# Performance work log

Hardware: AMD Instinct MI355X
Metric: run time of the kernel (lower is better)

## Reference

```python
import jax, jax.numpy as jnp
import numpy as np

H, D, G, P = 8, 64, 64, 3
ROPE_BASE = 10000.0

def _gelu(x):
    return jax.nn.gelu(x, approximate=False)  # torch nn.GELU default (erf)

def setup_inputs() -> dict:
    key = jax.random.key(0)
    ks = jax.random.split(key, 20)
    B, N, C = 2, 32768, 256
    inner = H * D
    s = 0.02
    inp = {
        'x': jax.random.normal(ks[0], (B, N, C), jnp.float32),
        'pos': jax.random.uniform(ks[1], (B, N, P), jnp.float32),
        'gumbel_u': jax.random.uniform(ks[2], (B, H, N, G), jnp.float32),
        'Wx': jax.random.normal(ks[3], (C, inner), jnp.float32) * s,
        'bx': jnp.zeros((inner,), jnp.float32),
        'W1': jax.random.normal(ks[4], (D, G), jnp.float32) * s,   # proj_temperature[0]
        'b1': jnp.zeros((G,), jnp.float32),
        'W2': jax.random.normal(ks[5], (G, 1), jnp.float32) * s,   # proj_temperature[2]
        'b2': jnp.zeros((1,), jnp.float32),
        'bias': jnp.full((1, H, 1, 1), 0.5, jnp.float32),
        'Wr': jax.random.normal(ks[6], (2 * P, D), jnp.float32) * s,  # rope_projection
        'br': jnp.zeros((D,), jnp.float32),
        'Ws': jax.random.normal(ks[7], (D, G), jnp.float32) * s,   # in_project_slice
        'bs': jnp.zeros((G,), jnp.float32),
        'Wq': jax.random.normal(ks[8], (D, D), jnp.float32) * s,
        'Wk': jax.random.normal(ks[9], (D, D), jnp.float32) * s,
        'Wv': jax.random.normal(ks[10], (D, D), jnp.float32) * s,
        'Wg1': jax.random.normal(ks[11], (2 * D, D), jnp.float32) * s,  # attn_gate[0]
        'bg1': jnp.zeros((D,), jnp.float32),
        'Wg2': jax.random.normal(ks[12], (D, D), jnp.float32) * s,      # attn_gate[2]
        'bg2': jnp.zeros((D,), jnp.float32),
        'Wo': jax.random.normal(ks[13], (inner, C), jnp.float32) * s,   # to_out
        'bo': jnp.zeros((C,), jnp.float32),
    }
    return inp

def reference(x, pos, gumbel_u, Wx, bx, W1, b1, W2, b2, bias, Wr, br, Ws, bs,
              Wq, Wk, Wv, Wg1, bg1, Wg2, bg2, Wo, bo):
    B, N, C = x.shape
    dt = x.dtype
    # project and split heads: [B,H,N,D]
    x_mid = (x @ Wx + bx).reshape(B, N, H, D).transpose(0, 2, 1, 3)
    # RoPE features: sin/cos of pos * inv_freq, projected to dim_head
    inv_freq = jnp.exp(-jnp.arange(P, dtype=dt) * jnp.log(jnp.asarray(ROPE_BASE, dt)) / P)
    ang = pos[..., :P] * inv_freq                                  # [B,N,P]
    rope_feat = jnp.concatenate([jnp.sin(ang), jnp.cos(ang)], -1)  # [B,N,2P]
    x_mid = x_mid + (rope_feat @ Wr + br)[:, None]                 # broadcast over heads
    # per-token temperature, clamped
    temp = _gelu(_gelu(x_mid @ W1 + b1) @ W2 + b2) + bias          # [B,H,N,1]
    temp = jnp.maximum(temp, 0.01)
    # gumbel-softmax slice weights (soft, hard=False)
    logits = x_mid @ Ws + bs                                       # [B,H,N,G]
    gnoise = -jnp.log(-jnp.log(gumbel_u + 1e-8) + 1e-8)
    sw = jax.nn.softmax((logits + gnoise) / temp, axis=-1)
    # pool N tokens into G slice tokens
    snorm = sw.sum(axis=2)                                         # [B,H,G]
    st = jnp.einsum('bhnc,bhng->bhgc', x_mid, sw) / (snorm + 1e-5)[..., None]
    # tiny SDPA over G learned tokens
    q, k, v = st @ Wq, st @ Wk, st @ Wv
    attn = jax.nn.softmax(jnp.einsum('bhgc,bhkc->bhgk', q, k) / jnp.sqrt(jnp.asarray(D, dt)), axis=-1)
    out_st = jnp.einsum('bhgk,bhkc->bhgc', attn, v)
    # sigmoid gate
    gate_in = jnp.concatenate([st, out_st], axis=-1)               # [B,H,G,2D]
    gate = jax.nn.sigmoid(jax.nn.silu(gate_in @ Wg1 + bg1) @ Wg2 + bg2)
    out_st = gate * out_st
    # broadcast slice tokens back to N tokens
    out_x = jnp.einsum('bhgc,bhng->bhnc', out_st, sw)
    out_x = out_x.transpose(0, 2, 1, 3).reshape(B, N, H * D)
    return out_x @ Wo + bo
```

## Files before the change

### kernel.cpp

```cpp
#include <hip/hip_runtime.h>
#include <math.h>

#define NSEQ 32768

using short8v = __attribute__((ext_vector_type(8))) short;
using f32x4   = __attribute__((ext_vector_type(4))) float;
#define MFMA16 __builtin_amdgcn_mfma_f32_16x16x32_bf16

__device__ __forceinline__ unsigned short f2bf(float f){
  union{float f; unsigned u;} v; v.f = f;
  return (unsigned short)((v.u + 0x7FFFu + ((v.u>>16)&1u))>>16);
}
__device__ __forceinline__ float bf2f(unsigned short h){
  union{unsigned u; float f;} v; v.u = ((unsigned)h)<<16; return v.f;
}
__device__ __forceinline__ void split2(float f, unsigned short* h, unsigned short* l){
  unsigned short hh = f2bf(f);
  *h = hh; *l = f2bf(f - bf2f(hh));
}
__device__ __forceinline__ float gelu_f(float x){
  return 0.5f*x*(1.f + erff(x*0.70710678118654752f));
}

__global__ __launch_bounds__(256) void k0_prep(const float* __restrict__ Wx,
    unsigned short* __restrict__ WxTH, unsigned short* __restrict__ WxTL)
{
  const int n = blockIdx.x;
  const int k = threadIdx.x;
  float v = Wx[(size_t)k*512 + n];
  unsigned short hh, ll; split2(v,&hh,&ll);
  WxTH[n*256+k]=hh; WxTL[n*256+k]=ll;
}

__global__ __launch_bounds__(256) void k0b_prep(
  const float* __restrict__ Wq, const float* __restrict__ Wk, const float* __restrict__ Wv,
  const float* __restrict__ Wg1, const float* __restrict__ Wg2, const float* __restrict__ Wo,
  const float* __restrict__ W1, const float* __restrict__ Ws,
  unsigned short* __restrict__ WqTH, unsigned short* __restrict__ WqTL,
  unsigned short* __restrict__ WkTH, unsigned short* __restrict__ WkTL,
  unsigned short* __restrict__ WvTH, unsigned short* __restrict__ WvTL,
  unsigned short* __restrict__ Wg1TH, unsigned short* __restrict__ Wg1TL,
  unsigned short* __restrict__ Wg2TH, unsigned short* __restrict__ Wg2TL,
  unsigned short* __restrict__ WoTH, unsigned short* __restrict__ WoTL,
  unsigned short* __restrict__ W1TH, unsigned short* __restrict__ W1TL,
  unsigned short* __restrict__ WsTH, unsigned short* __restrict__ WsTL)
{
  const int bx = blockIdx.x, t = threadIdx.x;
  unsigned short hh, ll;
  if (bx == 0){
    for (int i=0;i<16;i++){ int idx=i*256+t; int r=idx>>6, c=idx&63;
      split2(Wq[r*64+c],&hh,&ll); WqTH[c*64+r]=hh; WqTL[c*64+r]=ll;
      split2(Wk[r*64+c],&hh,&ll); WkTH[c*64+r]=hh; WkTL[c*64+r]=ll;
      split2(Wv[r*64+c],&hh,&ll); WvTH[c*64+r]=hh; WvTL[c*64+r]=ll;
    }
  } else if (bx == 1){
    for (int i=0;i<32;i++){ int idx=i*256+t; int r=idx>>6, c=idx&63;
      split2(Wg1[r*64+c],&hh,&ll); Wg1TH[c*128+r]=hh; Wg1TL[c*128+r]=ll;
    }
  } else if (bx == 2){
    for (int i=0;i<16;i++){ int idx=i*256+t; int r=idx>>6, c=idx&63;
      split2(Wg2[r*64+c],&hh,&ll); Wg2TH[c*64+r]=hh; Wg2TL[c*64+r]=ll;
      split2(W1[r*64+c],&hh,&ll);  W1TH[c*64+r]=hh;  W1TL[c*64+r]=ll;
      split2(Ws[r*64+c],&hh,&ll);  WsTH[c*64+r]=hh;  WsTL[c*64+r]=ll;
    }
  } else {
    int kb = (bx-3)*64;
    for (int i=0;i<64;i++){ int k = kb+i;
      split2(Wo[(size_t)k*256 + t],&hh,&ll);
      WoTH[(size_t)t*512 + k]=hh; WoTL[(size_t)t*512 + k]=ll;
    }
  }
}

__global__ __launch_bounds__(512,1) void k1_gemm_rope(
    const float* __restrict__ x, const float* __restrict__ pos,
    const unsigned short* __restrict__ WxTH, const unsigned short* __restrict__ WxTL,
    const float* __restrict__ bx,
    const float* __restrict__ Wr, const float* __restrict__ br,
    float* __restrict__ xmid)
{
  __shared__ unsigned short SA[2*128*128];
  __shared__ unsigned short SB[2*64*128];
  __shared__ float trig[128][8];
  const int tid = threadIdx.x;
  const int wave = tid>>6, lane = tid&63, l15 = lane&15, lq = lane>>4;
  const int m0 = blockIdx.x*128;

  if (tid < 128){
    int m = m0 + tid;
    float a0 = pos[m*3+0];
    float a1 = pos[m*3+1] * 0.046415888336127774f;
    float a2 = pos[m*3+2] * 0.002154434690031884f;
    trig[tid][0]=sinf(a0); trig[tid][1]=sinf(a1); trig[tid][2]=sinf(a2);
    trig[tid][3]=cosf(a0); trig[tid][4]=cosf(a1); trig[tid][5]=cosf(a2);
  }

  short8v aHr[8], aLr[8];
  {
    const int lm = tid>>2, lkq = (tid&3)*32;
    #pragma unroll
    for (int kh=0; kh<2; kh++){
      __syncthreads();
      const float* src = x + (size_t)(m0+lm)*256 + kh*128 + lkq;
      #pragma unroll
      for (int i=0;i<8;i++){
        float4 v = *(const float4*)(src + i*4);
        ushort4 hh, ll;
        split2(v.x,&hh.x,&ll.x); split2(v.y,&hh.y,&ll.y);
        split2(v.z,&hh.z,&ll.z); split2(v.w,&hh.w,&ll.w);
        int G = (lkq>>3) + (i>>1);
        int idx = lm*128 + (((G ^ (lm&15)))<<3) + ((i&1)<<2);
        *(ushort4*)&SA[idx] = hh;
        *(ushort4*)&SA[128*128 + idx] = ll;
      }
      __syncthreads();
      const int row = wave*16 + l15;
      #pragma unroll
      for (int ks=0; ks<4; ks++){
        int idx = row*128 + ((((ks<<2)+lq) ^ l15)<<3);
        aHr[kh*4+ks] = *(const short8v*)&SA[idx];
        aLr[kh*4+ks] = *(const short8v*)&SA[128*128 + idx];
      }
    }
  }

  float ropev[4][4];
  #pragma unroll
  for (int r=0;r<4;r++){
    int tk = wave*16 + lq*4 + r;
    float t0=trig[tk][0],t1=trig[tk][1],t2=trig[tk][2];
    float t3=trig[tk][3],t4=trig[tk][4],t5=trig[tk][5];
    #pragma unroll
    for (int j=0;j<4;j++){
      int d = j*16 + l15;
      float v = br[d];
      v = fmaf(t0, Wr[0*64+d], v);
      v = fmaf(t1, Wr[1*64+d], v);
      v = fmaf(t2, Wr[2*64+d], v);
      v = fmaf(t3, Wr[3*64+d], v);
      v = fmaf(t4, Wr[4*64+d], v);
      v = fmaf(t5, Wr[5*64+d], v);
      ropev[r][j] = v;
    }
  }

  const int bidx = m0 >> 15;
  const int nbase = (m0 & 32767) + wave*16 + lq*4;
  const int ln = tid>>3, lnkq = (tid&7)*16;

  for (int h=0; h<8; h++){
    f32x4 acc[4] = {};
    #pragma unroll
    for (int kh=0; kh<2; kh++){
      __syncthreads();
      {
        const unsigned short* sH = WxTH + (size_t)(h*64+ln)*256 + kh*128 + lnkq;
        const unsigned short* sL = WxTL + (size_t)(h*64+ln)*256 + kh*128 + lnkq;
        int g0 = lnkq>>3;
        int i0 = ln*128 + ((g0     ^ (ln&15))<<3);
        int i1 = ln*128 + (((g0+1) ^ (ln&15))<<3);
        *(uint4*)&SB[i0] = *(const uint4*)sH;
        *(uint4*)&SB[i1] = *(const uint4*)(sH+8);
        *(uint4*)&SB[64*128 + i0] = *(const uint4*)sL;
        *(uint4*)&SB[64*128 + i1] = *(const uint4*)(sL+8);
      }
      __syncthreads();
      #pragma unroll
      for (int ks=0; ks<4; ks++){
        short8v a_h = aHr[kh*4+ks], a_l = aLr[kh*4+ks];
        #pragma unroll
        for (int j=0;j<4;j++){
          int idx = (j*16+l15)*128 + ((((ks<<2)+lq) ^ l15)<<3);
          short8v b_h = *(const short8v*)&SB[idx];
          short8v b_l = *(const short8v*)&SB[64*128 + idx];
          acc[j] = MFMA16(a_h,b_h,acc[j],0,0,0);
          acc[j] = MFMA16(a_h,b_l,acc[j],0,0,0);
          acc[j] = MFMA16(a_l,b_h,acc[j],0,0,0);
        }
      }
    }
    #pragma unroll
    for (int j=0;j<4;j++){
      int col = j*16 + l15;
      float bxv = bx[h*64+col];
      #pragma unroll
      for (int r=0;r<4;r++){
        xmid[(((size_t)(bidx*8+h))*NSEQ + nbase + r)*64 + col] =
          acc[j][r] + bxv + ropev[r][j];
      }
    }
  }
}

__global__ __launch_bounds__(512,1) void k2_tile(
  const float* __restrict__ xmid, const float* __restrict__ gum,
  const unsigned short* __restrict__ W1TH, const unsigned short* __restrict__ W1TL,
  const float* __restrict__ b1,
  const float* __restrict__ W2, const float* __restrict__ b2,
  const float* __restrict__ biasp,
  const unsigned short* __restrict__ WsTH, const unsigned short* __restrict__ WsTL,
  const float* __restrict__ bs,
  unsigned* __restrict__ swT, float* __restrict__ part)
{
  __shared__ unsigned short XAh[128*72], XAl[128*72];
  __shared__ unsigned short XBh[64*128], XBl[64*128];
  __shared__ unsigned short W1h[64*72], W1l[64*72];
  __shared__ unsigned short Wsh[64*72], Wsl[64*72];
  __shared__ unsigned short swh[64*136], swl[64*136];
  __shared__ float snred[8*64];
  __shared__ float prm[200];

  const int tid = threadIdx.x;
  const int wave = tid>>6, lane = tid&63, l15 = lane&15, lq = lane>>4;
  const int bh = blockIdx.y, chunk = blockIdx.x, h = bh&7;
  const size_t rowbase = (size_t)bh*NSEQ;

  {
    const int g = tid>>3, c8 = (tid&7)*8;
    *(uint4*)&W1h[g*72+c8] = *(const uint4*)(W1TH + g*64 + c8);
    *(uint4*)&W1l[g*72+c8] = *(const uint4*)(W1TL + g*64 + c8);
    *(uint4*)&Wsh[g*72+c8] = *(const uint4*)(WsTH + g*64 + c8);
    *(uint4*)&Wsl[g*72+c8] = *(const uint4*)(WsTL + g*64 + c8);
  }
  if (tid<64){ prm[tid]=b1[tid]; prm[64+tid]=bs[tid]; prm[128+tid]=W2[tid]; }
  if (tid==64){ prm[192]=b2[0]; prm[193]=biasp[h]; }

  f32x4 acc2[2] = {};
  float snacc[4][4] = {};
  const int gt2 = wave>>1, dbase = (wave&1)*2;

  for (int sub=0; sub<4; ++sub){
    const int n0 = chunk*512 + sub*128;
    __syncthreads();
    {
      const int mq = (tid>>4)*4, dq = (tid&15)*4;
      const float* src = xmid + (rowbase + n0 + mq)*64 + dq;
      unsigned short hh[4][4], ll[4][4];
      #pragma unroll
      for (int i=0;i<4;i++){
        float4 v = *(const float4*)(src + i*64);
        split2(v.x,&hh[i][0],&ll[i][0]); split2(v.y,&hh[i][1],&ll[i][1]);
        split2(v.z,&hh[i][2],&ll[i][2]); split2(v.w,&hh[i][3],&ll[i][3]);
        ushort4 th; th.x=hh[i][0]; th.y=hh[i][1]; th.z=hh[i][2]; th.w=hh[i][3];
        ushort4 tl; tl.x=ll[i][0]; tl.y=ll[i][1]; tl.z=ll[i][2]; tl.w=ll[i][3];
        *(ushort4*)&XAh[(mq+i)*72 + dq] = th;
        *(ushort4*)&XAl[(mq+i)*72 + dq] = tl;
      }
      const int gm = mq>>3, mh = mq&7;
      #pragma unroll
      for (int j=0;j<4;j++){
        int d = dq+j;
        int base = d*128 + ((gm ^ (d&15))<<3) + mh;
        ushort4 th; th.x=hh[0][j]; th.y=hh[1][j]; th.z=hh[2][j]; th.w=hh[3][j];
        ushort4 tl; tl.x=ll[0][j]; tl.y=ll[1][j]; tl.z=ll[2][j]; tl.w=ll[3][j];
        *(ushort4*)&XBh[base] = th;
        *(ushort4*)&XBl[base] = tl;
      }
    }
    __syncthreads();

    const int mloc = wave*16 + l15;
    const float* grow = gum + (rowbase + n0 + mloc)*64;
    float4 gu[4];
    #pragma unroll
    for (int gt=0; gt<4; gt++) gu[gt] = *(const float4*)(grow + gt*16 + lq*4);

    f32x4 t1a[4] = {}, lga[4] = {};
    #pragma unroll
    for (int ks=0; ks<2; ks++){
      const int koff = ks*32 + lq*8;
      short8v xH = *(const short8v*)&XAh[(wave*16+l15)*72 + koff];
      short8v xL = *(const short8v*)&XAl[(wave*16+l15)*72 + koff];
      #pragma unroll
      for (int gt=0; gt<4; gt++){
        const int aoff = (gt*16+l15)*72 + koff;
        short8v wH = *(const short8v*)&W1h[aoff];
        short8v wL = *(const short8v*)&W1l[aoff];
        t1a[gt] = MFMA16(wH,xH,t1a[gt],0,0,0);
        t1a[gt] = MFMA16(wH,xL,t1a[gt],0,0,0);
        t1a[gt] = MFMA16(wL,xH,t1a[gt],0,0,0);
        short8v sH = *(const short8v*)&Wsh[aoff];
        short8v sL = *(const short8v*)&Wsl[aoff];
        lga[gt] = MFMA16(sH,xH,lga[gt],0,0,0);
        lga[gt] = MFMA16(sH,xL,lga[gt],0,0,0);
        lga[gt] = MFMA16(sL,xH,lga[gt],0,0,0);
      }
    }

    float p = 0.f;
    #pragma unroll
    for (int gt=0; gt<4; gt++)
      #pragma unroll
      for (int r=0;r<4;r++){
        int g = gt*16 + lq*4 + r;
        p += gelu_f(t1a[gt][r] + prm[g]) * prm[128+g];
      }
    p += __shfl_xor(p,16); p += __shfl_xor(p,32);
    float t2 = gelu_f(p + prm[192]);
    float rtemp = 1.f / fmaxf(t2 + prm[193], 0.01f);

    float z[4][4]; float mx = -1e30f;
    #pragma unroll
    for (int gt=0; gt<4; gt++){
      float guv[4] = {gu[gt].x, gu[gt].y, gu[gt].z, gu[gt].w};
      #pragma unroll
      for (int r=0;r<4;r++){
        int g = gt*16 + lq*4 + r;
        float gn = -__logf(-__logf(guv[r]+1e-8f)+1e-8f);
        float zz = (lga[gt][r] + prm[64+g] + gn)*rtemp;
        z[gt][r]=zz; mx = fmaxf(mx, zz);
      }
    }
    mx = fmaxf(mx, __shfl_xor(mx,16)); mx = fmaxf(mx, __shfl_xor(mx,32));
    float se = 0.f;
    #pragma unroll
    for (int gt=0; gt<4; gt++)
      #pragma unroll
      for (int r=0;r<4;r++){ float e = __expf(z[gt][r]-mx); z[gt][r]=e; se += e; }
    se += __shfl_xor(se,16); se += __shfl_xor(se,32);
    float inv = 1.f/se;
    #pragma unroll
    for (int gt=0; gt<4; gt++)
      #pragma unroll
      for (int r=0;r<4;r++){
        float swv = z[gt][r]*inv;
        snacc[gt][r] += swv;
        int g = gt*16 + lq*4 + r;
        unsigned short hh,ll; split2(swv,&hh,&ll);
        swh[g*136 + mloc] = hh; swl[g*136 + mloc] = ll;
      }
    __syncthreads();

    {
      const int g = tid>>3, mq = (tid&7)*16;
      #pragma unroll
      for (int i=0;i<4;i++){
        ushort4 hh = *(const ushort4*)&swh[g*136 + mq + i*4];
        ushort4 ll = *(const ushort4*)&swl[g*136 + mq + i*4];
        uint4 pk;
        pk.x = (unsigned)hh.x | ((unsigned)ll.x<<16);
        pk.y = (unsigned)hh.y | ((unsigned)ll.y<<16);
        pk.z = (unsigned)hh.z | ((unsigned)ll.z<<16);
        pk.w = (unsigned)hh.w | ((unsigned)ll.w<<16);
        *(uint4*)(swT + ((size_t)bh*64 + g)*NSEQ + n0 + mq + i*4) = pk;
      }
    }

    #pragma unroll
    for (int ks=0; ks<4; ks++){
      const int koff = ks*32 + lq*8;
      short8v aH = *(const short8v*)&swh[(gt2*16+l15)*136 + koff];
      short8v aL = *(const short8v*)&swl[(gt2*16+l15)*136 + koff];
      const int gran = ks*4 + lq;
      #pragma unroll
      for (int dt=0; dt<2; dt++){
        const int d = (dbase+dt)*16 + l15;
        const int boff = d*128 + ((gran ^ (d&15))<<3);
        short8v bH = *(const short8v*)&XBh[boff];
        short8v bL = *(const short8v*)&XBl[boff];
        acc2[dt] = MFMA16(aH,bH,acc2[dt],0,0,0);
        acc2[dt] = MFMA16(aH,bL,acc2[dt],0,0,0);
        acc2[dt] = MFMA16(aL,bH,acc2[dt],0,0,0);
      }
    }
  }

  float* pb = part + ((size_t)bh*64 + chunk)*4160;
  #pragma unroll
  for (int dt=0; dt<2; dt++)
    #pragma unroll
    for (int r=0;r<4;r++){
      int g = gt2*16 + lq*4 + r;
      int d = (dbase+dt)*16 + l15;
      pb[g*64 + d] = acc2[dt][r];
    }
  #pragma unroll
  for (int gt=0; gt<4; gt++)
    #pragma unroll
    for (int r=0;r<4;r++){
      float v = snacc[gt][r];
      v += __shfl_xor(v,1); v += __shfl_xor(v,2);
      v += __shfl_xor(v,4); v += __shfl_xor(v,8);
      if (l15==0) snred[wave*64 + gt*16 + lq*4 + r] = v;
    }
  __syncthreads();
  if (tid < 64){
    float s = 0.f;
    #pragma unroll
    for (int w=0; w<8; w++) s += snred[w*64 + tid];
    pb[4096 + tid] = s;
  }
}

__global__ __launch_bounds__(256) void k3a_reduce(
    const float* __restrict__ part, float* __restrict__ stred)
{
  const int bh = blockIdx.x;
  const int i = blockIdx.y*256 + threadIdx.x;
  if (i >= 4160) return;
  const float* pb = part + (size_t)bh*64*4160 + i;
  float s[8] = {};
  #pragma unroll 2
  for (int c=0; c<64; c+=8)
    #pragma unroll
    for (int j=0;j<8;j++) s[j] += pb[(size_t)(c+j)*4160];
  stred[bh*4160 + i] = ((s[0]+s[1])+(s[2]+s[3])) + ((s[4]+s[5])+(s[6]+s[7]));
}

__global__ __launch_bounds__(256) void k3b_slice(
    const float* __restrict__ stred,
    const unsigned short* __restrict__ WqTH, const unsigned short* __restrict__ WqTL,
    const unsigned short* __restrict__ WkTH, const unsigned short* __restrict__ WkTL,
    const unsigned short* __restrict__ WvTH, const unsigned short* __restrict__ WvTL,
    const unsigned short* __restrict__ Wg1TH, const unsigned short* __restrict__ Wg1TL,
    const unsigned short* __restrict__ Wg2TH, const unsigned short* __restrict__ Wg2TL,
    const unsigned short* __restrict__ WoTH, const unsigned short* __restrict__ WoTL,
    const float* __restrict__ bg1, const float* __restrict__ bg2,
    unsigned* __restrict__ MtP)
{
  __shared__ unsigned short stH[64*72], stL[64*72];
  __shared__ unsigned short qH[64*72],  qL[64*72];
  __shared__ unsigned short kH[64*72],  kL[64*72];
  __shared__ unsigned short vTH[64*72], vTL[64*72];
  __shared__ unsigned short pH[64*72],  pL[64*72];
  __shared__ unsigned short oH[64*72],  oL[64*72];
  __shared__ unsigned short h1H[64*72], h1L[64*72];
  __shared__ unsigned short gH[64*72],  gL[64*72];
  __shared__ float snl[64];

  const int tid = threadIdx.x;
  const int wave = tid>>6, lane = tid&63, l15 = lane&15, lq = lane>>4;
  const int bh = blockIdx.x, h = bh&7;
  const int grow = wave*16 + lq*4;

  if (tid < 64) snl[tid] = stred[bh*4160 + 4096 + tid] + 1e-5f;
  __syncthreads();
  {
    const int g = tid>>2, doff = (tid&3)*16;
    const float sn = snl[g];
    #pragma unroll
    for (int i=0;i<4;i++){
      float4 v = *(const float4*)(stred + bh*4160 + g*64 + doff + i*4);
      ushort4 hh, ll;
      split2(v.x/sn,&hh.x,&ll.x); split2(v.y/sn,&hh.y,&ll.y);
      split2(v.z/sn,&hh.z,&ll.z); split2(v.w/sn,&hh.w,&ll.w);
      *(ushort4*)&stH[g*72 + doff + i*4] = hh;
      *(ushort4*)&stL[g*72 + doff + i*4] = ll;
    }
  }
  __syncthreads();

  {
    f32x4 aq[4]={}, ak[4]={}, av[4]={};
    #pragma unroll
    for (int ks=0; ks<2; ks++){
      const int koff = ks*32 + lq*8;
// ... 133 lines not shown
        ga[dt]=MFMA16(aHf,bH,ga[dt],0,0,0); ga[dt]=MFMA16(aHf,bL,ga[dt],0,0,0); ga[dt]=MFMA16(aLf,bH,ga[dt],0,0,0);
      }
    }
    #pragma unroll
    for (int dt=0; dt<4; dt++){
      float bg = bg2[dt*16+l15];
      #pragma unroll
      for (int r=0;r<4;r++){
        float gate = 1.f/(1.f+__expf(-(ga[dt][r]+bg)));
        float gv = gate * os[dt][r];
        unsigned short hh,ll; split2(gv,&hh,&ll);
        gH[(grow+r)*72 + dt*16+l15]=hh; gL[(grow+r)*72 + dt*16+l15]=ll;
      }
    }
  }
  __syncthreads();

  {
    f32x4 mac[16] = {};
    #pragma unroll
    for (int ks=0; ks<2; ks++){
      const int koff = ks*32 + lq*8;
      short8v aHf = *(const short8v*)&gH[(wave*16+l15)*72 + koff];
      short8v aLf = *(const short8v*)&gL[(wave*16+l15)*72 + koff];
      #pragma unroll
      for (int ct=0; ct<16; ct++){
        const size_t boff = (size_t)(ct*16+l15)*512 + h*64 + koff;
        short8v bH = *(const short8v*)(WoTH+boff);
        short8v bL = *(const short8v*)(WoTL+boff);
        mac[ct]=MFMA16(aHf,bH,mac[ct],0,0,0); mac[ct]=MFMA16(aHf,bL,mac[ct],0,0,0); mac[ct]=MFMA16(aLf,bH,mac[ct],0,0,0);
      }
    }
    #pragma unroll
    for (int ct=0; ct<16; ct++)
      #pragma unroll
      for (int r=0;r<4;r++){
        unsigned short hh,ll; split2(mac[ct][r],&hh,&ll);
        MtP[(size_t)bh*16384 + (size_t)(ct*16+l15)*64 + grow + r] =
          (unsigned)hh | ((unsigned)ll<<16);
      }
  }
}

__global__ __launch_bounds__(256,2) void k4_out(
  const unsigned* __restrict__ swT, const unsigned* __restrict__ MtP,
  const float* __restrict__ bo, float* __restrict__ out)
{
  __shared__ unsigned short AH[64*72], AL[64*72];
  __shared__ unsigned short BH[128*72], BL[128*72];
  const int tid = threadIdx.x;
  const int wave = tid>>6, lane = tid&63, l15 = lane&15, lq = lane>>4;
  const int m0 = blockIdx.x*64, c0 = blockIdx.y*128;
  const int b = m0>>15, nn = m0 & 32767;
  f32x4 acc[8] = {};

  for (int hh=0; hh<8; hh++){
    const int bhh = b*8 + hh;
    __syncthreads();
    {
      const int g = tid>>2, mq = (tid&3)*16;
      const unsigned* src = swT + ((size_t)bhh*64 + g)*NSEQ + nn + mq;
      #pragma unroll
      for (int i=0;i<4;i++){
        uint4 pv = *(const uint4*)(src + i*4);
        unsigned u[4]={pv.x,pv.y,pv.z,pv.w};
        #pragma unroll
        for (int j=0;j<4;j++){
          int m = mq + i*4 + j;
          AH[m*72+g] = (unsigned short)(u[j] & 0xFFFFu);
          AL[m*72+g] = (unsigned short)(u[j] >> 16);
        }
      }
      const int c = tid>>1, gq = (tid&1)*32;
      const unsigned* bsrc = MtP + (size_t)bhh*16384 + (size_t)(c0+c)*64 + gq;
      #pragma unroll
      for (int i=0;i<8;i++){
        uint4 pv = *(const uint4*)(bsrc + i*4);
        ushort4 hh4, ll4;
        hh4.x=(unsigned short)(pv.x&0xFFFFu); ll4.x=(unsigned short)(pv.x>>16);
        hh4.y=(unsigned short)(pv.y&0xFFFFu); ll4.y=(unsigned short)(pv.y>>16);
        hh4.z=(unsigned short)(pv.z&0xFFFFu); ll4.z=(unsigned short)(pv.z>>16);
        hh4.w=(unsigned short)(pv.w&0xFFFFu); ll4.w=(unsigned short)(pv.w>>16);
        *(ushort4*)&BH[c*72 + gq + i*4] = hh4;
        *(ushort4*)&BL[c*72 + gq + i*4] = ll4;
      }
    }
    __syncthreads();
    #pragma unroll
    for (int ks=0; ks<2; ks++){
      const int koff = ks*32 + lq*8;
      short8v aH = *(const short8v*)&AH[(wave*16+l15)*72 + koff];
      short8v aL = *(const short8v*)&AL[(wave*16+l15)*72 + koff];
      #pragma unroll
      for (int ct=0; ct<8; ct++){
        short8v bH = *(const short8v*)&BH[(ct*16+l15)*72 + koff];
        short8v bL = *(const short8v*)&BL[(ct*16+l15)*72 + koff];
        acc[ct] = MFMA16(aH,bH,acc[ct],0,0,0);
        acc[ct] = MFMA16(aH,bL,acc[ct],0,0,0);
        acc[ct] = MFMA16(aL,bH,acc[ct],0,0,0);
      }
    }
  }
  #pragma unroll
  for (int ct=0; ct<8; ct++)
    #pragma unroll
    for (int r=0;r<4;r++){
      int c = c0 + ct*16 + l15;
      out[(size_t)(m0 + wave*16 + lq*4 + r)*256 + c] = acc[ct][r] + bo[c];
    }
}

extern "C" void kernel_launch(void* const* d_in, const int* in_sizes, int n_in,
                              void* d_out, int out_size, void* d_ws, size_t ws_size,
                              hipStream_t stream) {
  (void)in_sizes; (void)n_in; (void)out_size;
  const float* x    = (const float*)d_in[0];
  const float* pos  = (const float*)d_in[1];
  const float* gum  = (const float*)d_in[2];
  const float* Wx   = (const float*)d_in[3];
  const float* bx   = (const float*)d_in[4];
  const float* W1   = (const float*)d_in[5];
  const float* b1   = (const float*)d_in[6];
  const float* W2   = (const float*)d_in[7];
  const float* b2   = (const float*)d_in[8];
  const float* bias = (const float*)d_in[9];
  const float* Wr   = (const float*)d_in[10];
  const float* br   = (const float*)d_in[11];
  const float* Ws   = (const float*)d_in[12];
  const float* bs   = (const float*)d_in[13];
  const float* Wq   = (const float*)d_in[14];
  const float* Wk   = (const float*)d_in[15];
  const float* Wv   = (const float*)d_in[16];
  const float* Wg1  = (const float*)d_in[17];
  const float* bg1  = (const float*)d_in[18];
  const float* Wg2  = (const float*)d_in[19];
  const float* bg2  = (const float*)d_in[20];
  const float* Wo   = (const float*)d_in[21];
  const float* bo   = (const float*)d_in[22];
  float* out = (float*)d_out;

  float*    xmid  = (float*)d_ws;
  unsigned* swT   = (unsigned*)(xmid + (size_t)33554432);
  float*    partp = (float*)(swT + (size_t)33554432);
  float*    stred = partp + (size_t)4259840;
  unsigned short* WxTH = (unsigned short*)(stred + (size_t)66560);
  unsigned short* WxTL  = WxTH + (size_t)131072;
  unsigned short* WqTH  = WxTL + (size_t)131072;
  unsigned short* WqTL  = WqTH + 4096;
  unsigned short* WkTH  = WqTL + 4096;
  unsigned short* WkTL  = WkTH + 4096;
  unsigned short* WvTH  = WkTL + 4096;
  unsigned short* WvTL  = WvTH + 4096;
  unsigned short* Wg1TH = WvTL + 4096;
  unsigned short* Wg1TL = Wg1TH + 8192;
  unsigned short* Wg2TH = Wg1TL + 8192;
  unsigned short* Wg2TL = Wg2TH + 4096;
  unsigned short* WoTH  = Wg2TL + 4096;
  unsigned short* WoTL  = WoTH + (size_t)131072;
  unsigned short* W1TH  = WoTL + (size_t)131072;
  unsigned short* W1TL  = W1TH + 4096;
  unsigned short* WsTH  = W1TL + 4096;
  unsigned short* WsTL  = WsTH + 4096;
  unsigned* MtP = (unsigned*)partp;
  const size_t need = ((size_t)33554432*2 + 4259840 + 66560)*4 + (size_t)589824*2;
  if (ws_size < need) return;

  k0_prep<<<512, 256, 0, stream>>>(Wx, WxTH, WxTL);
  k0b_prep<<<11, 256, 0, stream>>>(Wq, Wk, Wv, Wg1, Wg2, Wo, W1, Ws,
      WqTH,WqTL,WkTH,WkTL,WvTH,WvTL,Wg1TH,Wg1TL,Wg2TH,Wg2TL,WoTH,WoTL,W1TH,W1TL,WsTH,WsTL);
  k1_gemm_rope<<<512, 512, 0, stream>>>(x, pos, WxTH, WxTL, bx, Wr, br, xmid);
  k2_tile<<<dim3(64,16), 512, 0, stream>>>(xmid, gum, W1TH, W1TL, b1, W2, b2, bias, WsTH, WsTL, bs, swT, partp);
  k3a_reduce<<<dim3(16,17), 256, 0, stream>>>(partp, stred);
  k3b_slice<<<16, 256, 0, stream>>>(stred, WqTH,WqTL,WkTH,WkTL,WvTH,WvTL,
      Wg1TH,Wg1TL,Wg2TH,Wg2TL,WoTH,WoTL, bg1, bg2, MtP);
  k4_out<<<dim3(1024,2), 256, 0, stream>>>(swT, MtP, bo, out);
}
```

Before: 418.0 us.

## Register-prefetch next tiles in slice-pool and output kernels; change XB swizzle

In the slice-pooling kernel and the k4_out output GEMM, global loads for the next sub-tile or head are issued into registers before the current tile's MFMA work. This hides global memory latency behind compute. The XB LDS swizzle also changes from an XOR pattern to an additive rotation to cut bank conflicts on the transposed stores and reads. The cost is more live registers, which may lower occupancy (k4_out has launch_bounds 256,2).

```diff
diff --git a/kernel.cpp b/kernel.cpp
--- a/kernel.cpp
+++ b/kernel.cpp
@@ -20,6 +20,9 @@
 }
 __device__ __forceinline__ float gelu_f(float x){
   return 0.5f*x*(1.f + erff(x*0.70710678118654752f));
+}
+__device__ __forceinline__ int xbslot(int g, int d){
+  return (g + (d>>2) + ((d&3)<<2)) & 15;
 }
 
 __global__ __launch_bounds__(256) void k0_prep(const float* __restrict__ Wx,
@@ -228,29 +231,40 @@
   f32x4 acc2[2] = {};
   float snacc[4][4] = {};
   const int gt2 = wave>>1, dbase = (wave&1)*2;
-
+  const int mqs = (tid>>4)*4, dqs = (tid&15)*4;
+  const int gms = mqs>>3, mhs = mqs&7;
+  const int mloc = wave*16 + l15;
+
+  float4 xm_c[4], gu_c[4];
+  {
+    const float* srcx = xmid + (rowbase + chunk*512 + mqs)*64 + dqs;
+    #pragma unroll
+    for (int i=0;i<4;i++) xm_c[i] = *(const float4*)(srcx + (size_t)i*64);
+    const float* srcg = gum + (rowbase + chunk*512 + mloc)*64;
+    #pragma unroll
+    for (int gt=0;gt<4;gt++) gu_c[gt] = *(const float4*)(srcg + gt*16 + lq*4);
+  }
+
+  #pragma unroll
   for (int sub=0; sub<4; ++sub){
     const int n0 = chunk*512 + sub*128;
     __syncthreads();
     {
-      const int mq = (tid>>4)*4, dq = (tid&15)*4;
-      const float* src = xmid + (rowbase + n0 + mq)*64 + dq;
       unsigned short hh[4][4], ll[4][4];
       #pragma unroll
       for (int i=0;i<4;i++){
-        float4 v = *(const float4*)(src + i*64);
+        float4 v = xm_c[i];
         split2(v.x,&hh[i][0],&ll[i][0]); split2(v.y,&hh[i][1],&ll[i][1]);
         split2(v.z,&hh[i][2],&ll[i][2]); split2(v.w,&hh[i][3],&ll[i][3]);
         ushort4 th; th.x=hh[i][0]; th.y=hh[i][1]; th.z=hh[i][2]; th.w=hh[i][3];
         ushort4 tl; tl.x=ll[i][0]; tl.y=ll[i][1]; tl.z=ll[i][2]; tl.w=ll[i][3];
-        *(ushort4*)&XAh[(mq+i)*72 + dq] = th;
-        *(ushort4*)&XAl[(mq+i)*72 + dq] = tl;
-      }
-      const int gm = mq>>3, mh = mq&7;
+        *(ushort4*)&XAh[(mqs+i)*72 + dqs] = th;
+        *(ushort4*)&XAl[(mqs+i)*72 + dqs] = tl;
+      }
       #pragma unroll
       for (int j=0;j<4;j++){
-        int d = dq+j;
-        int base = d*128 + ((gm ^ (d&15))<<3) + mh;
+        int d = dqs+j;
+        int base = d*128 + (xbslot(gms,d)<<3) + mhs;
         ushort4 th; th.x=hh[0][j]; th.y=hh[1][j]; th.z=hh[2][j]; th.w=hh[3][j];
         ushort4 tl; tl.x=ll[0][j]; tl.y=ll[1][j]; tl.z=ll[2][j]; tl.w=ll[3][j];
         *(ushort4*)&XBh[base] = th;
@@ -259,11 +273,15 @@
     }
     __syncthreads();
 
-    const int mloc = wave*16 + l15;
-    const float* grow = gum + (rowbase + n0 + mloc)*64;
-    float4 gu[4];
-    #pragma unroll
-    for (int gt=0; gt<4; gt++) gu[gt] = *(const float4*)(grow + gt*16 + lq*4);
+    float4 xm_n[4], gu_n[4];
+    if (sub<3){
+      const float* srcx = xmid + (rowbase + n0 + 128 + mqs)*64 + dqs;
+      #pragma unroll
+      for (int i=0;i<4;i++) xm_n[i] = *(const float4*)(srcx + (size_t)i*64);
+      const float* srcg = gum + (rowbase + n0 + 128 + mloc)*64;
+      #pragma unroll
+      for (int gt=0;gt<4;gt++) gu_n[gt] = *(const float4*)(srcg + gt*16 + lq*4);
+    }
 
     f32x4 t1a[4] = {}, lga[4] = {};
     #pragma unroll
@@ -302,7 +320,7 @@
     float z[4][4]; float mx = -1e30f;
     #pragma unroll
     for (int gt=0; gt<4; gt++){
-      float guv[4] = {gu[gt].x, gu[gt].y, gu[gt].z, gu[gt].w};
+      float guv[4] = {gu_c[gt].x, gu_c[gt].y, gu_c[gt].z, gu_c[gt].w};
       #pragma unroll
       for (int r=0;r<4;r++){
         int g = gt*16 + lq*4 + r;
@@ -355,13 +373,20 @@
       #pragma unroll
       for (int dt=0; dt<2; dt++){
         const int d = (dbase+dt)*16 + l15;
-        const int boff = d*128 + ((gran ^ (d&15))<<3);
+        const int boff = d*128 + (xbslot(gran,d)<<3);
         short8v bH = *(const short8v*)&XBh[boff];
         short8v bL = *(const short8v*)&XBl[boff];
         acc2[dt] = MFMA16(aH,bH,acc2[dt],0,0,0);
         acc2[dt] = MFMA16(aH,bL,acc2[dt],0,0,0);
         acc2[dt] = MFMA16(aL,bH,acc2[dt],0,0,0);
       }
+    }
+
+    if (sub<3){
+      #pragma unroll
+      for (int i=0;i<4;i++) xm_c[i] = xm_n[i];
+      #pragma unroll
+      for (int gt=0;gt<4;gt++) gu_c[gt] = gu_n[gt];
     }
   }
 
@@ -641,40 +666,58 @@
   const int wave = tid>>6, lane = tid&63, l15 = lane&15, lq = lane>>4;
   const int m0 = blockIdx.x*64, c0 = blockIdx.y*128;
   const int b = m0>>15, nn = m0 & 32767;
+  const int ga = tid>>2, mqa = (tid&3)*16;
+  const int cb = tid>>1, gqb = (tid&1)*32;
   f32x4 acc[8] = {};
 
+  uint4 pa_c[4], pb_c[8];
+  {
+    const unsigned* src = swT + ((size_t)(b*8)*64 + ga)*NSEQ + nn + mqa;
+    #pragma unroll
+    for (int i=0;i<4;i++) pa_c[i] = *(const uint4*)(src + i*4);
+    const unsigned* bsrc = MtP + (size_t)(b*8)*16384 + (size_t)(c0+cb)*64 + gqb;
+    #pragma unroll
+    for (int i=0;i<8;i++) pb_c[i] = *(const uint4*)(bsrc + i*4);
+  }
+
+  #pragma unroll
   for (int hh=0; hh<8; hh++){
-    const int bhh = b*8 + hh;
     __syncthreads();
     {
-      const int g = tid>>2, mq = (tid&3)*16;
-      const unsigned* src = swT + ((size_t)bhh*64 + g)*NSEQ + nn + mq;
       #pragma unroll
       for (int i=0;i<4;i++){
-        uint4 pv = *(const uint4*)(src + i*4);
-        unsigned u[4]={pv.x,pv.y,pv.z,pv.w};
+        unsigned u[4]={pa_c[i].x,pa_c[i].y,pa_c[i].z,pa_c[i].w};
         #pragma unroll
         for (int j=0;j<4;j++){
-          int m = mq + i*4 + j;
-          AH[m*72+g] = (unsigned short)(u[j] & 0xFFFFu);
-          AL[m*72+g] = (unsigned short)(u[j] >> 16);
+          int m = mqa + i*4 + j;
+          AH[m*72+ga] = (unsigned short)(u[j] & 0xFFFFu);
+          AL[m*72+ga] = (unsigned short)(u[j] >> 16);
         }
       }
-      const int c = tid>>1, gq = (tid&1)*32;
-      const unsigned* bsrc = MtP + (size_t)bhh*16384 + (size_t)(c0+c)*64 + gq;
       #pragma unroll
       for (int i=0;i<8;i++){
-        uint4 pv = *(const uint4*)(bsrc + i*4);
+        uint4 pv = pb_c[i];
         ushort4 hh4, ll4;
         hh4.x=(unsigned short)(pv.x&0xFFFFu); ll4.x=(unsigned short)(pv.x>>16);
         hh4.y=(unsigned short)(pv.y&0xFFFFu); ll4.y=(unsigned short)(pv.y>>16);
         hh4.z=(unsigned short)(pv.z&0xFFFFu); ll4.z=(unsigned short)(pv.z>>16);
         hh4.w=(unsigned short)(pv.w&0xFFFFu); ll4.w=(unsigned short)(pv.w>>16);
-        *(ushort4*)&BH[c*72 + gq + i*4] = hh4;
-        *(ushort4*)&BL[c*72 + gq + i*4] = ll4;
+        *(ushort4*)&BH[cb*72 + gqb + i*4] = hh4;
+        *(ushort4*)&BL[cb*72 + gqb + i*4] = ll4;
       }
     }
     __syncthreads();
+
+    uint4 pa_n[4], pb_n[8];
+    if (hh<7){
+      const unsigned* src = swT + ((size_t)(b*8+hh+1)*64 + ga)*NSEQ + nn + mqa;
+      #pragma unroll
+      for (int i=0;i<4;i++) pa_n[i] = *(const uint4*)(src + i*4);
+      const unsigned* bsrc = MtP + (size_t)(b*8+hh+1)*16384 + (size_t)(c0+cb)*64 + gqb;
+      #pragma unroll
+      for (int i=0;i<8;i++) pb_n[i] = *(const uint4*)(bsrc + i*4);
+    }
+
     #pragma unroll
     for (int ks=0; ks<2; ks++){
       const int koff = ks*32 + lq*8;
@@ -688,6 +731,13 @@
         acc[ct] = MFMA16(aH,bL,acc[ct],0,0,0);
         acc[ct] = MFMA16(aL,bH,acc[ct],0,0,0);
       }
+    }
+
+    if (hh<7){
+      #pragma unroll
+      for (int i=0;i<4;i++) pa_c[i] = pa_n[i];
+      #pragma unroll
+      for (int i=0;i<8;i++) pb_c[i] = pb_n[i];
     }
   }
   #pragma unroll
```

Result: slower. 550.4 us (+31.7%).

## Fuse projection GEMM with slice-weight tile kernel to drop xmid round trip

Applied to the files above, without the earlier changes.

Merges the x@Wx+RoPE kernel with the temperature/gumbel-softmax/slice-pooling kernel so each 128-token tile's per-head x_mid is packed as hi/lo bf16 pairs into LDS and consumed immediately. This removes the 128 MB fp32 xmid write and re-read through global memory. In exchange, each block now emits one partial per 128-token chunk instead of per 512 tokens, quadrupling the partial buffer and the reduction work in k3a. The fused kernel also uses a large LDS footprint and extra syncs per head.

```diff
diff --git a/kernel.cpp b/kernel.cpp
--- a/kernel.cpp
+++ b/kernel.cpp
@@ -17,6 +17,11 @@
 __device__ __forceinline__ void split2(float f, unsigned short* h, unsigned short* l){
   unsigned short hh = f2bf(f);
   *h = hh; *l = f2bf(f - bf2f(hh));
+}
+__device__ __forceinline__ unsigned pack2(float f){
+  unsigned short hh = f2bf(f);
+  union{float f; unsigned u;} rv; rv.f = f - bf2f(hh);
+  return (unsigned)hh | (rv.u & 0xFFFF0000u);
 }
 __device__ __forceinline__ float gelu_f(float x){
   return 0.5f*x*(1.f + erff(x*0.70710678118654752f));
@@ -72,27 +77,69 @@
   }
 }
 
-__global__ __launch_bounds__(512,1) void k1_gemm_rope(
+__global__ __launch_bounds__(512,1) void k12_fused(
     const float* __restrict__ x, const float* __restrict__ pos,
+    const float* __restrict__ gum,
     const unsigned short* __restrict__ WxTH, const unsigned short* __restrict__ WxTL,
     const float* __restrict__ bx,
     const float* __restrict__ Wr, const float* __restrict__ br,
-    float* __restrict__ xmid)
+    const unsigned short* __restrict__ W1TH, const unsigned short* __restrict__ W1TL,
+    const float* __restrict__ b1,
+    const float* __restrict__ W2, const float* __restrict__ b2,
+    const float* __restrict__ biasp,
+    const unsigned short* __restrict__ WsTH, const unsigned short* __restrict__ WsTL,
+    const float* __restrict__ bs,
+    unsigned* __restrict__ swT, float* __restrict__ part)
 {
-  __shared__ unsigned short SA[2*128*128];
-  __shared__ unsigned short SB[2*64*128];
-  __shared__ float trig[128][8];
+  __shared__ __attribute__((aligned(16))) unsigned char Lds[143136];
+  unsigned*       W1p  = (unsigned*)(Lds + 0);
+  unsigned*       Wsp  = (unsigned*)(Lds + 17408);
+  float*          trig = (float*)(Lds + 34816);
+  unsigned short* SB   = (unsigned short*)(Lds + 38912);
+  unsigned short* SA   = (unsigned short*)(Lds + 71680);
+  unsigned*       XT   = (unsigned*)(Lds + 71680);
+  unsigned*       swp  = (unsigned*)(Lds + 106496);
+  float*          snred= (float*)(Lds + 140288);
+  float*          prm  = (float*)(Lds + 142336);
+
   const int tid = threadIdx.x;
   const int wave = tid>>6, lane = tid&63, l15 = lane&15, lq = lane>>4;
   const int m0 = blockIdx.x*128;
+
+  {
+    const int g = tid>>3, c8 = (tid&7)*8;
+    ushort4 h0 = *(const ushort4*)(W1TH + g*64 + c8);
+    ushort4 h1 = *(const ushort4*)(W1TH + g*64 + c8 + 4);
+    ushort4 l0 = *(const ushort4*)(W1TL + g*64 + c8);
+    ushort4 l1 = *(const ushort4*)(W1TL + g*64 + c8 + 4);
+    uint4 p0, p1;
+    p0.x=(unsigned)h0.x|((unsigned)l0.x<<16); p0.y=(unsigned)h0.y|((unsigned)l0.y<<16);
+    p0.z=(unsigned)h0.z|((unsigned)l0.z<<16); p0.w=(unsigned)h0.w|((unsigned)l0.w<<16);
+    p1.x=(unsigned)h1.x|((unsigned)l1.x<<16); p1.y=(unsigned)h1.y|((unsigned)l1.y<<16);
+    p1.z=(unsigned)h1.z|((unsigned)l1.z<<16); p1.w=(unsigned)h1.w|((unsigned)l1.w<<16);
+    *(uint4*)&W1p[g*68 + c8]     = p0;
+    *(uint4*)&W1p[g*68 + c8 + 4] = p1;
+    h0 = *(const ushort4*)(WsTH + g*64 + c8);
+    h1 = *(const ushort4*)(WsTH + g*64 + c8 + 4);
+    l0 = *(const ushort4*)(WsTL + g*64 + c8);
+    l1 = *(const ushort4*)(WsTL + g*64 + c8 + 4);
+    p0.x=(unsigned)h0.x|((unsigned)l0.x<<16); p0.y=(unsigned)h0.y|((unsigned)l0.y<<16);
+    p0.z=(unsigned)h0.z|((unsigned)l0.z<<16); p0.w=(unsigned)h0.w|((unsigned)l0.w<<16);
+    p1.x=(unsigned)h1.x|((unsigned)l1.x<<16); p1.y=(unsigned)h1.y|((unsigned)l1.y<<16);
+    p1.z=(unsigned)h1.z|((unsigned)l1.z<<16); p1.w=(unsigned)h1.w|((unsigned)l1.w<<16);
+    *(uint4*)&Wsp[g*68 + c8]     = p0;
+    *(uint4*)&Wsp[g*68 + c8 + 4] = p1;
+  }
+  if (tid<64){ prm[tid]=b1[tid]; prm[64+tid]=bs[tid]; prm[128+tid]=W2[tid]; }
+  if (tid==64){ prm[192]=b2[0]; }
 
   if (tid < 128){
     int m = m0 + tid;
     float a0 = pos[m*3+0];
     float a1 = pos[m*3+1] * 0.046415888336127774f;
     float a2 = pos[m*3+2] * 0.002154434690031884f;
-    trig[tid][0]=sinf(a0); trig[tid][1]=sinf(a1); trig[tid][2]=sinf(a2);
-    trig[tid][3]=cosf(a0); trig[tid][4]=cosf(a1); trig[tid][5]=cosf(a2);
+    trig[tid*8+0]=sinf(a0); trig[tid*8+1]=sinf(a1); trig[tid*8+2]=sinf(a2);
+    trig[tid*8+3]=cosf(a0); trig[tid*8+4]=cosf(a1); trig[tid*8+5]=cosf(a2);
   }
 
   short8v aHr[8], aLr[8];
@@ -123,13 +170,14 @@
       }
     }
   }
+  __syncthreads();
 
   float ropev[4][4];
   #pragma unroll
   for (int r=0;r<4;r++){
     int tk = wave*16 + lq*4 + r;
-    float t0=trig[tk][0],t1=trig[tk][1],t2=trig[tk][2];
-    float t3=trig[tk][3],t4=trig[tk][4],t5=trig[tk][5];
+    float t0=trig[tk*8+0],t1=trig[tk*8+1],t2=trig[tk*8+2];
+    float t3=trig[tk*8+3],t4=trig[tk*8+4],t5=trig[tk*8+5];
     #pragma unroll
     for (int j=0;j<4;j++){
       int d = j*16 + l15;
@@ -145,10 +193,19 @@
   }
 
   const int bidx = m0 >> 15;
-  const int nbase = (m0 & 32767) + wave*16 + lq*4;
+  const int n0g = m0 & 32767;
+  const int chunkIdx = n0g >> 7;
+  const int mloc = wave*16 + l15;
   const int ln = tid>>3, lnkq = (tid&7)*16;
+  const int gt2 = wave>>1, dbase = (wave&1)*2;
 
   for (int h=0; h<8; h++){
+    const size_t rowb = ((size_t)(bidx*8+h))*NSEQ;
+    const float* grow = gum + (rowb + n0g + mloc)*64;
+    float4 gu[4];
+    #pragma unroll
+    for (int gt=0; gt<4; gt++) gu[gt] = *(const float4*)(grow + gt*16 + lq*4);
+
     f32x4 acc[4] = {};
     #pragma unroll
     for (int kh=0; kh<2; kh++){
@@ -179,108 +236,45 @@
         }
       }
     }
+    __syncthreads();
     #pragma unroll
     for (int j=0;j<4;j++){
       int col = j*16 + l15;
       float bxv = bx[h*64+col];
       #pragma unroll
-      for (int r=0;r<4;r++){
-        xmid[(((size_t)(bidx*8+h))*NSEQ + nbase + r)*64 + col] =
-          acc[j][r] + bxv + ropev[r][j];
-      }
-    }
-  }
-}
-
-__global__ __launch_bounds__(512,1) void k2_tile(
-  const float* __restrict__ xmid, const float* __restrict__ gum,
-  const unsigned short* __restrict__ W1TH, const unsigned short* __restrict__ W1TL,
-  const float* __restrict__ b1,
-  const float* __restrict__ W2, const float* __restrict__ b2,
-  const float* __restrict__ biasp,
-  const unsigned short* __restrict__ WsTH, const unsigned short* __restrict__ WsTL,
-  const float* __restrict__ bs,
-  unsigned* __restrict__ swT, float* __restrict__ part)
-{
-  __shared__ unsigned short XAh[128*72], XAl[128*72];
-  __shared__ unsigned short XBh[64*128], XBl[64*128];
-  __shared__ unsigned short W1h[64*72], W1l[64*72];
-  __shared__ unsigned short Wsh[64*72], Wsl[64*72];
-  __shared__ unsigned short swh[64*136], swl[64*136];
-  __shared__ float snred[8*64];
-  __shared__ float prm[200];
-
-  const int tid = threadIdx.x;
-  const int wave = tid>>6, lane = tid&63, l15 = lane&15, lq = lane>>4;
-  const int bh = blockIdx.y, chunk = blockIdx.x, h = bh&7;
-  const size_t rowbase = (size_t)bh*NSEQ;
-
-  {
-    const int g = tid>>3, c8 = (tid&7)*8;
-    *(uint4*)&W1h[g*72+c8] = *(const uint4*)(W1TH + g*64 + c8);
-    *(uint4*)&W1l[g*72+c8] = *(const uint4*)(W1TL + g*64 + c8);
-    *(uint4*)&Wsh[g*72+c8] = *(const uint4*)(WsTH + g*64 + c8);
-    *(uint4*)&Wsl[g*72+c8] = *(const uint4*)(WsTL + g*64 + c8);
-  }
-  if (tid<64){ prm[tid]=b1[tid]; prm[64+tid]=bs[tid]; prm[128+tid]=W2[tid]; }
-  if (tid==64){ prm[192]=b2[0]; prm[193]=biasp[h]; }
-
-  f32x4 acc2[2] = {};
-  float snacc[4][4] = {};
-  const int gt2 = wave>>1, dbase = (wave&1)*2;
-
-  for (int sub=0; sub<4; ++sub){
-    const int n0 = chunk*512 + sub*128;
+      for (int r=0;r<4;r++)
+        XT[(wave*16 + lq*4 + r)*68 + col] = pack2(acc[j][r] + bxv + ropev[r][j]);
+    }
     __syncthreads();
-    {
-      const int mq = (tid>>4)*4, dq = (tid&15)*4;
-      const float* src = xmid + (rowbase + n0 + mq)*64 + dq;
-      unsigned short hh[4][4], ll[4][4];
-      #pragma unroll
-      for (int i=0;i<4;i++){
-        float4 v = *(const float4*)(src + i*64);
-        split2(v.x,&hh[i][0],&ll[i][0]); split2(v.y,&hh[i][1],&ll[i][1]);
-        split2(v.z,&hh[i][2],&ll[i][2]); split2(v.w,&hh[i][3],&ll[i][3]);
-        ushort4 th; th.x=hh[i][0]; th.y=hh[i][1]; th.z=hh[i][2]; th.w=hh[i][3];
-        ushort4 tl; tl.x=ll[i][0]; tl.y=ll[i][1]; tl.z=ll[i][2]; tl.w=ll[i][3];
-        *(ushort4*)&XAh[(mq+i)*72 + dq] = th;
-        *(ushort4*)&XAl[(mq+i)*72 + dq] = tl;
-      }
-      const int gm = mq>>3, mh = mq&7;
-      #pragma unroll
-      for (int j=0;j<4;j++){
-        int d = dq+j;
-        int base = d*128 + ((gm ^ (d&15))<<3) + mh;
-        ushort4 th; th.x=hh[0][j]; th.y=hh[1][j]; th.z=hh[2][j]; th.w=hh[3][j];
-        ushort4 tl; tl.x=ll[0][j]; tl.y=ll[1][j]; tl.z=ll[2][j]; tl.w=ll[3][j];
-        *(ushort4*)&XBh[base] = th;
-        *(ushort4*)&XBl[base] = tl;
-      }
-    }
-    __syncthreads();
-
-    const int mloc = wave*16 + l15;
-    const float* grow = gum + (rowbase + n0 + mloc)*64;
-    float4 gu[4];
-    #pragma unroll
-    for (int gt=0; gt<4; gt++) gu[gt] = *(const float4*)(grow + gt*16 + lq*4);
 
     f32x4 t1a[4] = {}, lga[4] = {};
     #pragma unroll
     for (int ks=0; ks<2; ks++){
       const int koff = ks*32 + lq*8;
-      short8v xH = *(const short8v*)&XAh[(wave*16+l15)*72 + koff];
-      short8v xL = *(const short8v*)&XAl[(wave*16+l15)*72 + koff];
+      uint4 u0 = *(const uint4*)&XT[mloc*68 + koff];
+      uint4 u1 = *(const uint4*)&XT[mloc*68 + koff + 4];
+      unsigned pp[8] = {u0.x,u0.y,u0.z,u0.w,u1.x,u1.y,u1.z,u1.w};
+      short8v xH, xL;
+      #pragma unroll
+      for (int j=0;j<8;j++){ xH[j]=(short)(pp[j]&0xFFFFu); xL[j]=(short)(pp[j]>>16); }
       #pragma unroll
       for (int gt=0; gt<4; gt++){
-        const int aoff = (gt*16+l15)*72 + koff;
-        short8v wH = *(const short8v*)&W1h[aoff];
-        short8v wL = *(const short8v*)&W1l[aoff];
+        const int woff = (gt*16+l15)*68 + koff;
+        uint4 w0 = *(const uint4*)&W1p[woff];
+        uint4 w1 = *(const uint4*)&W1p[woff+4];
+        unsigned wp[8] = {w0.x,w0.y,w0.z,w0.w,w1.x,w1.y,w1.z,w1.w};
+        short8v wH, wL;
+        #pragma unroll
+        for (int j=0;j<8;j++){ wH[j]=(short)(wp[j]&0xFFFFu); wL[j]=(short)(wp[j]>>16); }
         t1a[gt] = MFMA16(wH,xH,t1a[gt],0,0,0);
         t1a[gt] = MFMA16(wH,xL,t1a[gt],0,0,0);
         t1a[gt] = MFMA16(wL,xH,t1a[gt],0,0,0);
-        short8v sH = *(const short8v*)&Wsh[aoff];
-        short8v sL = *(const short8v*)&Wsl[aoff];
+        uint4 s0 = *(const uint4*)&Wsp[woff];
+        uint4 s1 = *(const uint4*)&Wsp[woff+4];
+        unsigned sp[8] = {s0.x,s0.y,s0.z,s0.w,s1.x,s1.y,s1.z,s1.w};
+        short8v sH, sL;
+        #pragma unroll
+        for (int j=0;j<8;j++){ sH[j]=(short)(sp[j]&0xFFFFu); sL[j]=(short)(sp[j]>>16); }
         lga[gt] = MFMA16(sH,xH,lga[gt],0,0,0);
         lga[gt] = MFMA16(sH,xL,lga[gt],0,0,0);
         lga[gt] = MFMA16(sL,xH,lga[gt],0,0,0);
@@ -297,7 +291,7 @@
       }
     p += __shfl_xor(p,16); p += __shfl_xor(p,32);
     float t2 = gelu_f(p + prm[192]);
-    float rtemp = 1.f / fmaxf(t2 + prm[193], 0.01f);
+    float rtemp = 1.f / fmaxf(t2 + biasp[h], 0.01f);
 
     float z[4][4]; float mx = -1e30f;
     #pragma unroll
@@ -319,15 +313,16 @@
       for (int r=0;r<4;r++){ float e = __expf(z[gt][r]-mx); z[gt][r]=e; se += e; }
     se += __shfl_xor(se,16); se += __shfl_xor(se,32);
     float inv = 1.f/se;
+    float snacc[4][4];
     #pragma unroll
     for (int gt=0; gt<4; gt++)
       #pragma unroll
       for (int r=0;r<4;r++){
         float swv = z[gt][r]*inv;
-        snacc[gt][r] += swv;
+        snacc[gt][r] = swv;
         int g = gt*16 + lq*4 + r;
         unsigned short hh,ll; split2(swv,&hh,&ll);
-        swh[g*136 + mloc] = hh; swl[g*136 + mloc] = ll;
+        swp[g*132 + mloc] = (unsigned)hh | ((unsigned)ll<<16);
       }
     __syncthreads();
 
@@ -335,60 +330,62 @@
       const int g = tid>>3, mq = (tid&7)*16;
       #pragma unroll
       for (int i=0;i<4;i++){
-        ushort4 hh = *(const ushort4*)&swh[g*136 + mq + i*4];
-        ushort4 ll = *(const ushort4*)&swl[g*136 + mq + i*4];
-        uint4 pk;
-        pk.x = (unsigned)hh.x | ((unsigned)ll.x<<16);
-        pk.y = (unsigned)hh.y | ((unsigned)ll.y<<16);
-        pk.z = (unsigned)hh.z | ((unsigned)ll.z<<16);
-        pk.w = (unsigned)hh.w | ((unsigned)ll.w<<16);
-        *(uint4*)(swT + ((size_t)bh*64 + g)*NSEQ + n0 + mq + i*4) = pk;
-      }
-    }
-
+        uint4 v = *(const uint4*)&swp[g*132 + mq + i*4];
+        *(uint4*)(swT + ((size_t)(bidx*8+h)*64 + g)*NSEQ + n0g + mq + i*4) = v;
+      }
+    }
+
+    f32x4 acc2[2] = {};
     #pragma unroll
     for (int ks=0; ks<4; ks++){
       const int koff = ks*32 + lq*8;
-      short8v aH = *(const short8v*)&swh[(gt2*16+l15)*136 + koff];
-      short8v aL = *(const short8v*)&swl[(gt2*16+l15)*136 + koff];
-      const int gran = ks*4 + lq;
+      uint4 a0 = *(const uint4*)&swp[(gt2*16+l15)*132 + koff];
+      uint4 a1 = *(const uint4*)&swp[(gt2*16+l15)*132 + koff + 4];
+      unsigned ap[8] = {a0.x,a0.y,a0.z,a0.w,a1.x,a1.y,a1.z,a1.w};
+      short8v aH, aL;
+      #pragma unroll
+      for (int j=0;j<8;j++){ aH[j]=(short)(ap[j]&0xFFFFu); aL[j]=(short)(ap[j]>>16); }
       #pragma unroll
       for (int dt=0; dt<2; dt++){
         const int d = (dbase+dt)*16 + l15;
-        const int boff = d*128 + ((gran ^ (d&15))<<3);
-        short8v bH = *(const short8v*)&XBh[boff];
-        short8v bL = *(const short8v*)&XBl[boff];
+        short8v bH, bL;
+        #pragma unroll
+        for (int j=0;j<8;j++){
+          unsigned u = XT[(koff+j)*68 + d];
+          bH[j] = (short)(u & 0xFFFFu);
+          bL[j] = (short)(u >> 16);
+        }
         acc2[dt] = MFMA16(aH,bH,acc2[dt],0,0,0);
         acc2[dt] = MFMA16(aH,bL,acc2[dt],0,0,0);
         acc2[dt] = MFMA16(aL,bH,acc2[dt],0,0,0);
       }
     }
-  }
-
-  float* pb = part + ((size_t)bh*64 + chunk)*4160;
-  #pragma unroll
-  for (int dt=0; dt<2; dt++)
-    #pragma unroll
-    for (int r=0;r<4;r++){
-      int g = gt2*16 + lq*4 + r;
-      int d = (dbase+dt)*16 + l15;
-      pb[g*64 + d] = acc2[dt][r];
-    }
-  #pragma unroll
-  for (int gt=0; gt<4; gt++)
-    #pragma unroll
-    for (int r=0;r<4;r++){
-      float v = snacc[gt][r];
-      v += __shfl_xor(v,1); v += __shfl_xor(v,2);
-      v += __shfl_xor(v,4); v += __shfl_xor(v,8);
-      if (l15==0) snred[wave*64 + gt*16 + lq*4 + r] = v;
-    }
-  __syncthreads();
-  if (tid < 64){
-    float s = 0.f;
-    #pragma unroll
-    for (int w=0; w<8; w++) s += snred[w*64 + tid];
-    pb[4096 + tid] = s;
+
+    float* pb = part + ((size_t)(bidx*8+h)*256 + chunkIdx)*4160;
+    #pragma unroll
+    for (int dt=0; dt<2; dt++)
+      #pragma unroll
+      for (int r=0;r<4;r++){
+        int g = gt2*16 + lq*4 + r;
+        int d = (dbase+dt)*16 + l15;
+        pb[g*64 + d] = acc2[dt][r];
+      }
+    #pragma unroll
+    for (int gt=0; gt<4; gt++)
+      #pragma unroll
+      for (int r=0;r<4;r++){
+        float v = snacc[gt][r];
+        v += __shfl_xor(v,1); v += __shfl_xor(v,2);
+        v += __shfl_xor(v,4); v += __shfl_xor(v,8);
+        if (l15==0) snred[wave*64 + gt*16 + lq*4 + r] = v;
+      }
+    __syncthreads();
+    if (tid < 64){
+      float s = 0.f;
+      #pragma unroll
+      for (int w=0; w<8; w++) s += snred[w*64 + tid];
+      pb[4096 + tid] = s;
+    }
   }
 }
 
@@ -398,10 +395,9 @@
   const int bh = blockIdx.x;
   const int i = blockIdx.y*256 + threadIdx.x;
   if (i >= 4160) return;
-  const float* pb = part + (size_t)bh*64*4160 + i;
+  const float* pb = part + (size_t)bh*256*4160 + i;
   float s[8] = {};
-  #pragma unroll 2
-  for (int c=0; c<64; c+=8)
+  for (int c=0; c<256; c+=8)
     #pragma unroll
     for (int j=0;j<8;j++) s[j] += pb[(size_t)(c+j)*4160];
   stred[bh*4160 + i] = ((s[0]+s[1])+(s[2]+s[3])) + ((s[4]+s[5])+(s[6]+s[7]));
@@ -728,10 +724,9 @@
   const float* bo   = (const float*)d_in[22];
   float* out = (float*)d_out;
 
-  float*    xmid  = (float*)d_ws;
-  unsigned* swT   = (unsigned*)(xmid + (size_t)33554432);
+  unsigned* swT   = (unsigned*)d_ws;
   float*    partp = (float*)(swT + (size_t)33554432);
-  float*    stred = partp + (size_t)4259840;
+  float*    stred = partp + (size_t)17039360;
   unsigned short* WxTH = (unsigned short*)(stred + (size_t)66560);
   unsigned short* WxTL  = WxTH + (size_t)131072;
   unsigned short* WqTH  = WxTL + (size_t)131072;
@@ -751,14 +746,14 @@
   unsigned short* WsTH  = W1TL + 4096;
   unsigned short* WsTL  = WsTH + 4096;
   unsigned* MtP = (unsigned*)partp;
-  const size_t need = ((size_t)33554432*2 + 4259840 + 66560)*4 + (size_t)589824*2;
+  const size_t need = ((size_t)33554432 + 17039360 + 66560)*4 + (size_t)589824*2;
   if (ws_size < need) return;
 
   k0_prep<<<512, 256, 0, stream>>>(Wx, WxTH, WxTL);
   k0b_prep<<<11, 256, 0, stream>>>(Wq, Wk, Wv, Wg1, Wg2, Wo, W1, Ws,
       WqTH,WqTL,WkTH,WkTL,WvTH,WvTL,Wg1TH,Wg1TL,Wg2TH,Wg2TL,WoTH,WoTL,W1TH,W1TL,WsTH,WsTL);
-  k1_gemm_rope<<<512, 512, 0, stream>>>(x, pos, WxTH, WxTL, bx, Wr, br, xmid);
-  k2_tile<<<dim3(64,16), 512, 0, stream>>>(xmid, gum, W1TH, W1TL, b1, W2, b2, bias, WsTH, WsTL, bs, swT, partp);
+  k12_fused<<<512, 512, 0, stream>>>(x, pos, gum, WxTH, WxTL, bx, Wr, br,
+      W1TH, W1TL, b1, W2, b2, bias, WsTH, WsTL, bs, swT, partp);
   k3a_reduce<<<dim3(16,17), 256, 0, stream>>>(partp, stred);
   k3b_slice<<<16, 256, 0, stream>>>(stred, WqTH,WqTL,WkTH,WkTL,WvTH,WvTL,
       Wg1TH,Wg1TL,Wg2TH,Wg2TL,WoTH,WoTL, bg1, bg2, MtP);
```

Result: slower. 474.8 us (+13.6%).
